# Performance work log

Measured on AMD Instinct MI355X. Metric: run time of the kernel, lower is better.

The kernel has to match this reference:

```python
import jax, jax.numpy as jnp
import numpy as np

T, B, H = 1024, 4096, 4  # time steps, students, BKT params (l,f,g,s)


def setup_inputs() -> dict:
    key = jax.random.key(0)
    ks = jax.random.split(key, 6)
    # binary correctness sequences, like the original BKT data
    x = (jax.random.uniform(ks[0], (T, B, 1)) < 0.5).astype(jnp.float32)
    y = (jax.random.uniform(ks[1], (T, B, 1)) < 0.5).astype(jnp.float32)
    s = 1.0 / np.sqrt(H)  # torch nn.RNN default init: U(-1/sqrt(H), 1/sqrt(H))
    W_ih = jax.random.uniform(ks[2], (H, 1), minval=-s, maxval=s, dtype=jnp.float32)
    W_hh = jax.random.uniform(ks[3], (H, H), minval=-s, maxval=s, dtype=jnp.float32)
    b_ih = jax.random.uniform(ks[4], (H,), minval=-s, maxval=s, dtype=jnp.float32)
    b_hh = jax.random.uniform(ks[5], (H,), minval=-s, maxval=s, dtype=jnp.float32)
    prior = jnp.array([0.1], dtype=jnp.float32)
    return {"x": x, "y": y, "prior": prior, "W_ih": W_ih, "W_hh": W_hh,
            "b_ih": b_ih, "b_hh": b_hh}


def _bce(p, y):
    # torch BCELoss clamps log terms at -100
    logp = jnp.maximum(jnp.log(p), -100.0)
    log1mp = jnp.maximum(jnp.log(1.0 - p), -100.0)
    return -(y * logp + (1.0 - y) * log1mp).mean()


def _forward(x, y, prior, W_ih, W_hh, b_ih, b_hh):
    Bn = x.shape[1]
    Hn = W_hh.shape[0]

    # --- Elman RNN (tanh), seq-first, h0 = 0 ---
    def rnn_step(h, x_t):  # x_t: [B,1], h: [B,H]
        h = jnp.tanh(x_t @ W_ih.T + b_ih + h @ W_hh.T + b_hh)
        return h, h

    h0 = jnp.zeros((Bn, Hn), dtype=x.dtype)
    _, output = jax.lax.scan(rnn_step, h0, x)  # [T,B,H]
    params = (output + 1.0) / 2.0  # map tanh output into (0,1)

    # --- sequential nonlinear BKT latent recurrence ---
    latent0 = jnp.broadcast_to(jax.nn.sigmoid(prior), (Bn, 1)).astype(x.dtype)

    def bkt_step(latent, inp):
        p_t, y_t = inp  # p_t: [B,H], y_t: [B,1]
        l, f, g, s = p_t[:, 0:1], p_t[:, 1:2], p_t[:, 2:3], p_t[:, 3:4]
        correct = latent * (1 - s) + (1 - latent) * g
        k_t1 = latent * (1 - s) / (latent * (1 - s) + (1 - latent) * g)
        k_t0 = latent * s / (latent * s + (1 - latent) * (1 - g))
        m_t = k_t1 * correct + k_t0 * (1 - correct)
        next_latent = m_t * (1 - f) + (1 - m_t) * l
        return next_latent, (correct, next_latent, _bce(correct, y_t))

    _, (corrects, latents, losses) = jax.lax.scan(bkt_step, latent0, (params, y))
    loss = losses.mean()  # sum of per-step BCE / T
    return corrects, latents, loss


def reference(x, y, prior, W_ih, W_hh, b_ih, b_hh):
    return _forward(x, y, prior, W_ih, W_hh, b_ih, b_hh)
```

## Files before the change

### kernel.cpp

```cpp
#include <hip/hip_runtime.h>

#define TT 1024
#define BB 4096
#define CHUNK 128
#define WARM 320
#define NC (TT / CHUNK)

template<int CTRL>
__device__ __forceinline__ float qperm(float v) {
    int i = __builtin_bit_cast(int, v);
    i = __builtin_amdgcn_mov_dpp(i, CTRL, 0xF, 0xF, true);
    return __builtin_bit_cast(float, i);
}

__launch_bounds__(64, 2)
__global__ void bkt_rnn_k(const float* __restrict__ x,
                          const float* __restrict__ y,
                          const float* __restrict__ prior,
                          const float* __restrict__ W_ih,
                          const float* __restrict__ W_hh,
                          const float* __restrict__ b_ih,
                          const float* __restrict__ b_hh,
                          float* __restrict__ out,
                          float* __restrict__ lossPart)
{
    __shared__ unsigned char xls[(WARM + CHUNK) * 16];
    __shared__ unsigned char yls[CHUNK * 16];
    __shared__ float cbuf[512];
    __shared__ float nbuf[512];

    const int lane = threadIdx.x;
    const int j  = lane & 3;
    const int le = lane >> 2;
    const int c  = blockIdx.x >> 8;
    const int eg = blockIdx.x & 255;
    const int e0 = eg * 16;

    const int t_out0   = c * CHUNK;
    const int t_start  = (t_out0 > WARM) ? (t_out0 - WARM) : 0;
    const int nwarm    = t_out0 - t_start;
    const int nsteps   = nwarm + CHUNK;

    for (int idx = lane; idx < nsteps * 16; idx += 64) {
        int t = t_start + (idx >> 4);
        xls[idx] = (x[(size_t)t * BB + e0 + (idx & 15)] != 0.0f);
    }
    for (int idx = lane; idx < CHUNK * 16; idx += 64) {
        int t = t_out0 + (idx >> 4);
        yls[idx] = (y[(size_t)t * BB + e0 + (idx & 15)] != 0.0f);
    }
    __syncthreads();

    const float S = 2.8853900817779268f;
    const float wj0 = W_hh[j * 4 + (j ^ 0)];
    const float wj1 = W_hh[j * 4 + (j ^ 1)];
    const float wj2 = W_hh[j * 4 + (j ^ 2)];
    const float wj3 = W_hh[j * 4 + (j ^ 3)];
    const float v0 = -2.f * S * wj0, v1 = -2.f * S * wj1;
    const float v2 = -2.f * S * wj2, v3 = -2.f * S * wj3;
    const float base0 = S * (b_ih[j] + b_hh[j] + wj0 + wj1 + wj2 + wj3);
    const float base1 = base0 + S * W_ih[j];

    float latent = 1.0f / (1.0f + __builtin_amdgcn_exp2f(-1.4426950408889634f * prior[0]));
    float rq0 = 0.5f, rq1 = 0.5f, rq2 = 0.5f, rq3 = 0.5f;
    float lossAcc = 0.0f;

    #pragma unroll 8
    for (int s = 0; s < nwarm; ++s) {
        float cxb = xls[(s << 4) | le] ? base1 : base0;
        float z = fmaf(rq0, v0, cxb);
        z = fmaf(rq1, v1, z);
        z = fmaf(rq2, v2, z);
        z = fmaf(rq3, v3, z);
        float ex = __builtin_amdgcn_exp2f(z);
        float r  = __builtin_amdgcn_rcpf(ex + 1.0f);
        rq0 = r;
        rq1 = qperm<0xB1>(r);
        rq2 = qperm<0x4E>(r);
        rq3 = qperm<0x1B>(r);
        float u1 = rq0 + rq1;
        latent = fmaf(latent, u1 - 1.0f, 1.0f - rq0);
    }

    const int rr = lane >> 2;
    const int cc = lane & 3;
    for (int g = 0; g < 4; ++g) {
        const int sbase = nwarm + g * 32;
        #pragma unroll
        for (int i = 0; i < 32; ++i) {
            float cxb = xls[((sbase + i) << 4) | le] ? base1 : base0;
            float z = fmaf(rq0, v0, cxb);
            z = fmaf(rq1, v1, z);
            z = fmaf(rq2, v2, z);
            z = fmaf(rq3, v3, z);
            float ex = __builtin_amdgcn_exp2f(z);
            float r  = __builtin_amdgcn_rcpf(ex + 1.0f);
            rq0 = r;
            rq1 = qperm<0xB1>(r);
            rq2 = qperm<0x4E>(r);
            rq3 = qperm<0x1B>(r);
            float u2   = rq2 + rq3;
            float corr = fmaf(latent, u2 - 1.0f, 1.0f - rq2);
            float u1   = rq0 + rq1;
            float nl   = fmaf(latent, u1 - 1.0f, 1.0f - rq0);
            if (j == 0) { cbuf[i * 16 + le] = corr; nbuf[i * 16 + le] = nl; }
            latent = nl;
        }
        __syncthreads();
        float4 c0 = *(const float4*)&cbuf[rr * 16 + cc * 4];
        float4 c1 = *(const float4*)&cbuf[(rr + 16) * 16 + cc * 4];
        float4 n0 = *(const float4*)&nbuf[rr * 16 + cc * 4];
        float4 n1 = *(const float4*)&nbuf[(rr + 16) * 16 + cc * 4];
        __syncthreads();

        const int tg = t_out0 + g * 32;
        float* cO = out + (size_t)(tg + rr) * BB + e0 + cc * 4;
        *(float4*)cO = c0;
        *(float4*)(cO + (size_t)16 * BB) = c1;
        float* lO = cO + (size_t)TT * BB;
        *(float4*)lO = n0;
        *(float4*)(lO + (size_t)16 * BB) = n1;

        auto bce = [&](float cv, int i, int el) {
            float lp = yls[((g * 32 + i) << 4) | el] ? cv : (1.0f - cv);
            float lg = __builtin_amdgcn_logf(lp) * 0.6931471805599453f;
            lossAcc += fmaxf(lg, -100.0f);
        };
        bce(c0.x, rr,      cc * 4 + 0); bce(c0.y, rr,      cc * 4 + 1);
        bce(c0.z, rr,      cc * 4 + 2); bce(c0.w, rr,      cc * 4 + 3);
        bce(c1.x, rr + 16, cc * 4 + 0); bce(c1.y, rr + 16, cc * 4 + 1);
        bce(c1.z, rr + 16, cc * 4 + 2); bce(c1.w, rr + 16, cc * 4 + 3);
    }

    #pragma unroll
    for (int o = 32; o >= 1; o >>= 1) lossAcc += __shfl_xor(lossAcc, o, 64);
    if (lane == 0) lossPart[blockIdx.x] = lossAcc;
}

__global__ void reduce_k(const float* __restrict__ part, float* __restrict__ loss) {
    float acc = 0.f;
    for (int i = threadIdx.x; i < 2048; i += 256) acc += part[i];
    #pragma unroll
    for (int o = 32; o >= 1; o >>= 1) acc += __shfl_xor(acc, o, 64);
    __shared__ float w[4];
    if ((threadIdx.x & 63) == 0) w[threadIdx.x >> 6] = acc;
    __syncthreads();
    if (threadIdx.x == 0) {
        float t = w[0] + w[1] + w[2] + w[3];
        *loss = t * (-1.0f / ((float)TT * (float)BB));
    }
}

extern "C" void kernel_launch(void* const* d_in, const int* in_sizes, int n_in,
                              void* d_out, int out_size, void* d_ws, size_t ws_size,
                              hipStream_t stream) {
    const float* x    = (const float*)d_in[0];
    const float* y    = (const float*)d_in[1];
    const float* pr   = (const float*)d_in[2];
    const float* W_ih = (const float*)d_in[3];
    const float* W_hh = (const float*)d_in[4];
    const float* b_ih = (const float*)d_in[5];
    const float* b_hh = (const float*)d_in[6];
    float* out = (float*)d_out;
    float* lossPart = (float*)d_ws;

    bkt_rnn_k<<<256 * NC, 64, 0, stream>>>(x, y, pr, W_ih, W_hh, b_ih, b_hh, out, lossPart);
    reduce_k<<<1, 256, 0, stream>>>(lossPart, out + 2 * (size_t)TT * BB);
}
```

Measured before the change: 140.7 us.

## Interleave four independent student groups per wave with smaller time chunks

```diff
diff --git a/kernel.cpp b/kernel.cpp
--- a/kernel.cpp
+++ b/kernel.cpp
@@ -2,9 +2,10 @@
 
 #define TT 1024
 #define BB 4096
-#define CHUNK 128
+#define CHUNK 64
 #define WARM 320
-#define NC (TT / CHUNK)
+#define NCH (TT / CHUNK)
+#define NSTEPMAX (WARM + CHUNK)
 
 template<int CTRL>
 __device__ __forceinline__ float qperm(float v) {
@@ -13,7 +14,7 @@
     return __builtin_bit_cast(float, i);
 }
 
-__launch_bounds__(64, 2)
+__launch_bounds__(64, 1)
 __global__ void bkt_rnn_k(const float* __restrict__ x,
                           const float* __restrict__ y,
                           const float* __restrict__ prior,
@@ -24,30 +25,39 @@
                           float* __restrict__ out,
                           float* __restrict__ lossPart)
 {
-    __shared__ unsigned char xls[(WARM + CHUNK) * 16];
-    __shared__ unsigned char yls[CHUNK * 16];
-    __shared__ float cbuf[512];
-    __shared__ float nbuf[512];
+    __shared__ unsigned char xls[NSTEPMAX * 64];
+    __shared__ unsigned char yls[CHUNK * 64];
+    __shared__ float cbuf[16 * 64];
+    __shared__ float nbuf[16 * 64];
 
     const int lane = threadIdx.x;
     const int j  = lane & 3;
     const int le = lane >> 2;
-    const int c  = blockIdx.x >> 8;
-    const int eg = blockIdx.x & 255;
-    const int e0 = eg * 16;
+    const int c  = blockIdx.x >> 6;
+    const int eg = blockIdx.x & 63;
+    const int e0 = eg * 64;
 
-    const int t_out0   = c * CHUNK;
-    const int t_start  = (t_out0 > WARM) ? (t_out0 - WARM) : 0;
-    const int nwarm    = t_out0 - t_start;
-    const int nsteps   = nwarm + CHUNK;
+    const int t_out0  = c * CHUNK;
+    const int nwarm   = (t_out0 > WARM) ? WARM : t_out0;
+    const int t_start = t_out0 - nwarm;
+    const int nsteps  = nwarm + CHUNK;
 
-    for (int idx = lane; idx < nsteps * 16; idx += 64) {
-        int t = t_start + (idx >> 4);
-        xls[idx] = (x[(size_t)t * BB + e0 + (idx & 15)] != 0.0f);
+    const int cc4 = (lane & 15) * 4;
+    const int rof = lane >> 4;
+
+    for (int rb = 0; rb < nsteps; rb += 4) {
+        const int r = rb + rof;
+        float4 v = *(const float4*)&x[(size_t)(t_start + r) * BB + e0 + cc4];
+        unsigned w = (v.x != 0.f ? 1u : 0u) | (v.y != 0.f ? 0x100u : 0u)
+                   | (v.z != 0.f ? 0x10000u : 0u) | (v.w != 0.f ? 0x1000000u : 0u);
+        *(unsigned*)&xls[r * 64 + cc4] = w;
     }
-    for (int idx = lane; idx < CHUNK * 16; idx += 64) {
-        int t = t_out0 + (idx >> 4);
-        yls[idx] = (y[(size_t)t * BB + e0 + (idx & 15)] != 0.0f);
+    for (int rb = 0; rb < CHUNK; rb += 4) {
+        const int r = rb + rof;
+        float4 v = *(const float4*)&y[(size_t)(t_out0 + r) * BB + e0 + cc4];
+        unsigned w = (v.x != 0.f ? 1u : 0u) | (v.y != 0.f ? 0x100u : 0u)
+                   | (v.z != 0.f ? 0x10000u : 0u) | (v.w != 0.f ? 0x1000000u : 0u);
+        *(unsigned*)&yls[r * 64 + cc4] = w;
     }
     __syncthreads();
 
@@ -61,75 +71,78 @@
     const float base0 = S * (b_ih[j] + b_hh[j] + wj0 + wj1 + wj2 + wj3);
     const float base1 = base0 + S * W_ih[j];
 
-    float latent = 1.0f / (1.0f + __builtin_amdgcn_exp2f(-1.4426950408889634f * prior[0]));
-    float rq0 = 0.5f, rq1 = 0.5f, rq2 = 0.5f, rq3 = 0.5f;
-    float lossAcc = 0.0f;
+    const float sig = 1.0f / (1.0f + __builtin_amdgcn_exp2f(-1.4426950408889634f * prior[0]));
+    float rq0[4], rq1[4], rq2[4], rq3[4], lat[4];
+    #pragma unroll
+    for (int n = 0; n < 4; ++n) { rq0[n] = rq1[n] = rq2[n] = rq3[n] = 0.5f; lat[n] = sig; }
 
-    #pragma unroll 8
+    #pragma unroll 4
     for (int s = 0; s < nwarm; ++s) {
-        float cxb = xls[(s << 4) | le] ? base1 : base0;
-        float z = fmaf(rq0, v0, cxb);
-        z = fmaf(rq1, v1, z);
-        z = fmaf(rq2, v2, z);
-        z = fmaf(rq3, v3, z);
-        float ex = __builtin_amdgcn_exp2f(z);
-        float r  = __builtin_amdgcn_rcpf(ex + 1.0f);
-        rq0 = r;
-        rq1 = qperm<0xB1>(r);
-        rq2 = qperm<0x4E>(r);
-        rq3 = qperm<0x1B>(r);
-        float u1 = rq0 + rq1;
-        latent = fmaf(latent, u1 - 1.0f, 1.0f - rq0);
+        #pragma unroll
+        for (int n = 0; n < 4; ++n) {
+            float cxb = xls[s * 64 + n * 16 + le] ? base1 : base0;
+            float t0 = fmaf(rq0[n], v0, cxb);
+            float u  = rq3[n] * v3;
+            float t1 = fmaf(rq1[n], v1, u);
+            float t2 = fmaf(rq2[n], v2, t0);
+            float z  = t1 + t2;
+            float ex = __builtin_amdgcn_exp2f(z);
+            float r  = __builtin_amdgcn_rcpf(ex + 1.0f);
+            rq0[n] = r;
+            rq1[n] = qperm<0xB1>(r);
+            rq2[n] = qperm<0x4E>(r);
+            rq3[n] = qperm<0x1B>(r);
+            lat[n] = fmaf(lat[n], (rq0[n] + rq1[n]) - 1.0f, 1.0f - rq0[n]);
+        }
     }
 
-    const int rr = lane >> 2;
-    const int cc = lane & 3;
+    float lossAcc = 0.0f;
     for (int g = 0; g < 4; ++g) {
-        const int sbase = nwarm + g * 32;
-        #pragma unroll
-        for (int i = 0; i < 32; ++i) {
-            float cxb = xls[((sbase + i) << 4) | le] ? base1 : base0;
-            float z = fmaf(rq0, v0, cxb);
-            z = fmaf(rq1, v1, z);
-            z = fmaf(rq2, v2, z);
-            z = fmaf(rq3, v3, z);
-            float ex = __builtin_amdgcn_exp2f(z);
-            float r  = __builtin_amdgcn_rcpf(ex + 1.0f);
-            rq0 = r;
-            rq1 = qperm<0xB1>(r);
-            rq2 = qperm<0x4E>(r);
-            rq3 = qperm<0x1B>(r);
-            float u2   = rq2 + rq3;
-            float corr = fmaf(latent, u2 - 1.0f, 1.0f - rq2);
-            float u1   = rq0 + rq1;
-            float nl   = fmaf(latent, u1 - 1.0f, 1.0f - rq0);
-            if (j == 0) { cbuf[i * 16 + le] = corr; nbuf[i * 16 + le] = nl; }
-            latent = nl;
+        #pragma unroll 4
+        for (int i = 0; i < 16; ++i) {
+            const int s = nwarm + g * 16 + i;
+            #pragma unroll
+            for (int n = 0; n < 4; ++n) {
+                float cxb = xls[s * 64 + n * 16 + le] ? base1 : base0;
+                float t0 = fmaf(rq0[n], v0, cxb);
+                float u  = rq3[n] * v3;
+                float t1 = fmaf(rq1[n], v1, u);
+                float t2 = fmaf(rq2[n], v2, t0);
+                float z  = t1 + t2;
+                float ex = __builtin_amdgcn_exp2f(z);
+                float r  = __builtin_amdgcn_rcpf(ex + 1.0f);
+                rq0[n] = r;
+                rq1[n] = qperm<0xB1>(r);
+                rq2[n] = qperm<0x4E>(r);
+                rq3[n] = qperm<0x1B>(r);
+                float corr = fmaf(lat[n], (rq2[n] + rq3[n]) - 1.0f, 1.0f - rq2[n]);
+                float nl   = fmaf(lat[n], (rq0[n] + rq1[n]) - 1.0f, 1.0f - rq0[n]);
+                if (j == 0) {
+                    cbuf[i * 64 + n * 16 + le] = corr;
+                    nbuf[i * 64 + n * 16 + le] = nl;
+                }
+                lat[n] = nl;
+            }
         }
         __syncthreads();
-        float4 c0 = *(const float4*)&cbuf[rr * 16 + cc * 4];
-        float4 c1 = *(const float4*)&cbuf[(rr + 16) * 16 + cc * 4];
-        float4 n0 = *(const float4*)&nbuf[rr * 16 + cc * 4];
-        float4 n1 = *(const float4*)&nbuf[(rr + 16) * 16 + cc * 4];
+        const int tg = t_out0 + g * 16;
+        #pragma unroll
+        for (int k = 0; k < 4; ++k) {
+            const int row = k * 4 + rof;
+            float4 cv = *(const float4*)&cbuf[row * 64 + cc4];
+            float4 nv = *(const float4*)&nbuf[row * 64 + cc4];
+            float* cO = out + (size_t)(tg + row) * BB + e0 + cc4;
+            *(float4*)cO = cv;
+            *(float4*)(cO + (size_t)TT * BB) = nv;
+            unsigned yw = *(const unsigned*)&yls[(g * 16 + row) * 64 + cc4];
+            auto bce = [&](float cvv, unsigned bit) {
+                float lp = bit ? cvv : (1.0f - cvv);
+                lossAcc += fmaxf(__builtin_amdgcn_logf(lp) * 0.6931471805599453f, -100.0f);
+            };
+            bce(cv.x, yw & 0xFFu);     bce(cv.y, yw & 0xFF00u);
+            bce(cv.z, yw & 0xFF0000u); bce(cv.w, yw & 0xFF000000u);
+        }
         __syncthreads();
-
-        const int tg = t_out0 + g * 32;
-        float* cO = out + (size_t)(tg + rr) * BB + e0 + cc * 4;
-        *(float4*)cO = c0;
-        *(float4*)(cO + (size_t)16 * BB) = c1;
-        float* lO = cO + (size_t)TT * BB;
-        *(float4*)lO = n0;
-        *(float4*)(lO + (size_t)16 * BB) = n1;
-
-        auto bce = [&](float cv, int i, int el) {
-            float lp = yls[((g * 32 + i) << 4) | el] ? cv : (1.0f - cv);
-            float lg = __builtin_amdgcn_logf(lp) * 0.6931471805599453f;
-            lossAcc += fmaxf(lg, -100.0f);
-        };
-        bce(c0.x, rr,      cc * 4 + 0); bce(c0.y, rr,      cc * 4 + 1);
-        bce(c0.z, rr,      cc * 4 + 2); bce(c0.w, rr,      cc * 4 + 3);
-        bce(c1.x, rr + 16, cc * 4 + 0); bce(c1.y, rr + 16, cc * 4 + 1);
-        bce(c1.z, rr + 16, cc * 4 + 2); bce(c1.w, rr + 16, cc * 4 + 3);
     }
 
     #pragma unroll
@@ -139,7 +152,7 @@
 
 __global__ void reduce_k(const float* __restrict__ part, float* __restrict__ loss) {
     float acc = 0.f;
-    for (int i = threadIdx.x; i < 2048; i += 256) acc += part[i];
+    for (int i = threadIdx.x; i < 1024; i += 256) acc += part[i];
     #pragma unroll
     for (int o = 32; o >= 1; o >>= 1) acc += __shfl_xor(acc, o, 64);
     __shared__ float w[4];
@@ -164,6 +177,6 @@
     float* out = (float*)d_out;
     float* lossPart = (float*)d_ws;
 
-    bkt_rnn_k<<<256 * NC, 64, 0, stream>>>(x, y, pr, W_ih, W_hh, b_ih, b_hh, out, lossPart);
+    bkt_rnn_k<<<NCH * 64, 64, 0, stream>>>(x, y, pr, W_ih, W_hh, b_ih, b_hh, out, lossPart);
     reduce_k<<<1, 256, 0, stream>>>(lossPart, out + 2 * (size_t)TT * BB);
 }
```

New measurement: 173.0 us. 1.23x slower.
